# Kernel tuning notes

Hardware: AMD Instinct MI355X
Metric: run time of the kernel (lower is better)

## Reference

```python
import jax, jax.numpy as jnp
import numpy as np

N, T, V = 256, 70, 64
B, H, C = 6, 1024, 4  # n_blocks, n_internal_units, n_class
SPECTRAL_RADIUS = 0.99
INPUT_SCALING = 0.2


def setup_inputs() -> dict:
    key = jax.random.key(0)
    k1, k2, k3, k4 = jax.random.split(key, 4)
    X = jax.random.normal(k1, (N, T, V), dtype=jnp.float32)
    # spectral-radius-normalized reservoir weights (circular law: rho(G/sqrt(H)) ~ 1)
    W_res = jax.random.normal(k2, (B, H, H), dtype=jnp.float32) * (SPECTRAL_RADIUS / jnp.sqrt(H).astype(jnp.float32))
    # +/-1 Bernoulli input weights scaled by input_scaling
    W_in = jnp.sign(jax.random.normal(k3, (B, H, V), dtype=jnp.float32)) * INPUT_SCALING
    W_lin = jax.random.normal(k4, (T, C, B * H), dtype=jnp.float32) * 0.02
    b_lin = jnp.zeros((T, C), dtype=jnp.float32)
    return {"X": X, "W_res": W_res, "W_in": W_in, "W_lin": W_lin, "b_lin": b_lin}


def reference(X, W_res, W_in, W_lin, b_lin):
    # Echo state recurrence: s_t = tanh(W_res @ s_{t-1} + W_in @ x_t), per block
    # (leak=None, noise_level=0.0, n_drop=0 as in module defaults)
    n, t_len, v = X.shape
    b, h, _ = W_res.shape

    def step(s, x_t):  # s: [B,N,H], x_t: [N,V]
        pre = jnp.einsum('bij,bnj->bni', W_res, s) + jnp.einsum('bhv,nv->bnh', W_in, x_t)
        s_new = jnp.tanh(pre)
        return s_new, s_new

    s0 = jnp.zeros((b, n, h), dtype=X.dtype)
    _, states = jax.lax.scan(step, s0, jnp.swapaxes(X, 0, 1))  # [T,B,N,H]

    # per-timestep features: concat blocks -> [T,N,B*H]
    feats = jnp.transpose(states, (0, 2, 1, 3)).reshape(t_len, n, b * h)
    # per-timestep linear heads
    logits = jnp.einsum('tnf,tcf->tnc', feats, W_lin) + b_lin[:, None, :]  # [T,N,C]
    preds = jnp.argmax(logits, axis=-1)  # [T,N], matches forward()'s class_dict
    return logits, preds
```

## Files before the change

### kernel.cpp

```cpp
#include <hip/hip_runtime.h>
#include <stdint.h>


typedef _Float16 f16;
typedef _Float16 f16x8 __attribute__((ext_vector_type(8)));
typedef float floatx4 __attribute__((ext_vector_type(4)));

#define N_TOT 256
#define T_TOT 70
#define V_TOT 64
#define B_TOT 6
#define H_TOT 1024
#define C_TOT 4
#define F_TOT (B_TOT * H_TOT)
#define G_TOT 192
#define LDA 72
#define LO_SCALE 4096.0f
#define LO_INV   (1.0f / 4096.0f)

union H8 { f16 h[8]; uint4 v; };

__global__ __launch_bounds__(256)
void split_f32(const float* __restrict__ src, f16* __restrict__ hi,
               f16* __restrict__ lo, int n)
{
    const int i = (blockIdx.x * 256 + threadIdx.x) * 8;
    if (i + 8 > n) return;
    const float4 a = *(const float4*)&src[i];
    const float4 b = *(const float4*)&src[i + 4];
    const float x[8] = {a.x, a.y, a.z, a.w, b.x, b.y, b.z, b.w};
    H8 H, L;
#pragma unroll
    for (int j = 0; j < 8; ++j) {
        const f16 h = (f16)x[j];
        H.h[j] = h;
        L.h[j] = (f16)((x[j] - (float)h) * LO_SCALE);
    }
    *(uint4*)&hi[i] = H.v;
    *(uint4*)&lo[i] = L.v;
}

__global__ __launch_bounds__(256)
void head_reduce(const float* __restrict__ part,
                 const float* __restrict__ b_lin,
                 float* __restrict__ logits,
                 float* __restrict__ preds)
{
    const int t = blockIdx.x;
    const int n = threadIdx.x;

    float a0 = b_lin[t * C_TOT + 0];
    float a1 = b_lin[t * C_TOT + 1];
    float a2 = b_lin[t * C_TOT + 2];
    float a3 = b_lin[t * C_TOT + 3];

    const float* p = part + (((size_t)t * G_TOT) * N_TOT + n) * C_TOT;
    for (int g = 0; g < G_TOT; ++g) {
        const float4 v = *(const float4*)&p[(size_t)g * N_TOT * C_TOT];
        a0 += v.x; a1 += v.y; a2 += v.z; a3 += v.w;
    }

    float4 o = {a0, a1, a2, a3};
    *(float4*)&logits[((size_t)t * N_TOT + n) * C_TOT] = o;

    int arg = 0;
    float best = a0;
    if (a1 > best) { best = a1; arg = 1; }
    if (a2 > best) { best = a2; arg = 2; }
    if (a3 > best) { best = a3; arg = 3; }
    preds[(size_t)t * N_TOT + n] = (float)arg;
}

__global__ __launch_bounds__(256)
void esn_step_fused(const f16* __restrict__ Xhi,   const f16* __restrict__ Xlo,
                    const f16* __restrict__ Whi,   const f16* __restrict__ Wlo,
                    const f16* __restrict__ Wihi,  const f16* __restrict__ Wilo,
                    const f16* __restrict__ shi_p, const f16* __restrict__ slo_p,
                    f16* __restrict__ shi_n,       f16* __restrict__ slo_n,
                    const float* __restrict__ W_lin, float* __restrict__ part,
                    int t, int first)
{
    __shared__ f16 As_hi[64 * LDA];
    __shared__ f16 As_lo[64 * LDA];
    __shared__ f16 Bs_hi[32 * LDA];
    __shared__ f16 Bs_lo[32 * LDA];

    const int id  = blockIdx.x;
    const int b   = id >> 7;
    const int rem = id & 127;
    const int mt  = rem >> 5;
    const int it  = rem & 31;

    const int tid  = threadIdx.x;
    const int wm   = tid >> 6;
    const int lane = tid & 63;
    const int l16  = lane & 15;
    const int oct  = lane >> 4;

    const int ra = tid >> 2;
    const int ca = (tid & 3) << 4;
    const int rb = tid >> 3;
    const int cb = (tid & 7) << 3;

    floatx4 acc[2], accl[2];
#pragma unroll
    for (int j = 0; j < 2; ++j) { acc[j] = (floatx4)(0.0f); accl[j] = (floatx4)(0.0f); }

    if (!first) {
        const f16* Ah = shi_p + (size_t)(b * N_TOT + mt * 64 + ra) * H_TOT + ca;
        const f16* Al = slo_p + (size_t)(b * N_TOT + mt * 64 + ra) * H_TOT + ca;
        const f16* Bh = Whi   + (size_t)(b * H_TOT + it * 32 + rb) * H_TOT + cb;
        const f16* Bl = Wlo   + (size_t)(b * H_TOT + it * 32 + rb) * H_TOT + cb;

        uint4 pah0, pah1, pal0, pal1, pbh, pbl;
#define LOAD_CHUNK(J0)                                   \
        do {                                             \
            pah0 = *(const uint4*)&Ah[(J0) + 0];         \
            pah1 = *(const uint4*)&Ah[(J0) + 8];         \
            pal0 = *(const uint4*)&Al[(J0) + 0];         \
            pal1 = *(const uint4*)&Al[(J0) + 8];         \
            pbh  = *(const uint4*)&Bh[(J0)];             \
            pbl  = *(const uint4*)&Bl[(J0)];             \
        } while (0)

        LOAD_CHUNK(0);
        for (int kc = 0; kc < 16; ++kc) {
            if (kc) __syncthreads();
            *(uint4*)&As_hi[ra * LDA + ca]     = pah0;
            *(uint4*)&As_hi[ra * LDA + ca + 8] = pah1;
            *(uint4*)&As_lo[ra * LDA + ca]     = pal0;
            *(uint4*)&As_lo[ra * LDA + ca + 8] = pal1;
            *(uint4*)&Bs_hi[rb * LDA + cb]     = pbh;
            *(uint4*)&Bs_lo[rb * LDA + cb]     = pbl;
            __syncthreads();
            if (kc < 15) LOAD_CHUNK((kc + 1) * 64);

#pragma unroll
            for (int kk = 0; kk < 64; kk += 32) {
                const int ar = (wm * 16 + l16) * LDA + kk + oct * 8;
                const f16x8 ah = *(const f16x8*)&As_hi[ar];
                const f16x8 al = *(const f16x8*)&As_lo[ar];
#pragma unroll
                for (int nf = 0; nf < 2; ++nf) {
                    const int br = (nf * 16 + l16) * LDA + kk + oct * 8;
                    const f16x8 bh = *(const f16x8*)&Bs_hi[br];
                    const f16x8 bl = *(const f16x8*)&Bs_lo[br];
                    acc[nf]  = __builtin_amdgcn_mfma_f32_16x16x32_f16(ah, bh, acc[nf], 0, 0, 0);
                    accl[nf] = __builtin_amdgcn_mfma_f32_16x16x32_f16(ah, bl, accl[nf], 0, 0, 0);
                    accl[nf] = __builtin_amdgcn_mfma_f32_16x16x32_f16(al, bh, accl[nf], 0, 0, 0);
                }
            }
        }
#undef LOAD_CHUNK
        __syncthreads();
    }

    {
        const size_t xb = ((size_t)(mt * 64 + ra) * T_TOT + t) * V_TOT + ca;
        *(uint4*)&As_hi[ra * LDA + ca]     = *(const uint4*)&Xhi[xb];
        *(uint4*)&As_hi[ra * LDA + ca + 8] = *(const uint4*)&Xhi[xb + 8];
        *(uint4*)&As_lo[ra * LDA + ca]     = *(const uint4*)&Xlo[xb];
        *(uint4*)&As_lo[ra * LDA + ca + 8] = *(const uint4*)&Xlo[xb + 8];
        const size_t wb = (size_t)(b * H_TOT + it * 32 + rb) * V_TOT + cb;
        *(uint4*)&Bs_hi[rb * LDA + cb] = *(const uint4*)&Wihi[wb];
        *(uint4*)&Bs_lo[rb * LDA + cb] = *(const uint4*)&Wilo[wb];
        __syncthreads();
#pragma unroll
        for (int kk = 0; kk < 64; kk += 32) {
            const int ar = (wm * 16 + l16) * LDA + kk + oct * 8;
            const f16x8 ah = *(const f16x8*)&As_hi[ar];
            const f16x8 al = *(const f16x8*)&As_lo[ar];
#pragma unroll
            for (int nf = 0; nf < 2; ++nf) {
                const int br = (nf * 16 + l16) * LDA + kk + oct * 8;
                const f16x8 bh = *(const f16x8*)&Bs_hi[br];
                const f16x8 bl = *(const f16x8*)&Bs_lo[br];
                acc[nf]  = __builtin_amdgcn_mfma_f32_16x16x32_f16(ah, bh, acc[nf], 0, 0, 0);
                accl[nf] = __builtin_amdgcn_mfma_f32_16x16x32_f16(ah, bl, accl[nf], 0, 0, 0);
                accl[nf] = __builtin_amdgcn_mfma_f32_16x16x32_f16(al, bh, accl[nf], 0, 0, 0);
            }
        }
    }

    const int nbase = mt * 64;
    const int ibase = it * 32;

    const float* wl = W_lin + (size_t)t * C_TOT * F_TOT + b * H_TOT + ibase;
    float w[4][2];
#pragma unroll
    for (int c = 0; c < 4; ++c)
#pragma unroll
        for (int nf = 0; nf < 2; ++nf)
            w[c][nf] = wl[(size_t)c * F_TOT + nf * 16 + l16];

    float sval[2][4];
#pragma unroll
    for (int nf = 0; nf < 2; ++nf)
#pragma unroll
        for (int r = 0; r < 4; ++r) {
            const int m  = wm * 16 + oct * 4 + r;
            const int ii = nf * 16 + l16;
            const float s = tanhf(acc[nf][r] + accl[nf][r] * LO_INV);
            sval[nf][r] = s;
            const f16 h = (f16)s;
            const size_t oidx = (size_t)(b * N_TOT + nbase + m) * H_TOT + ibase + ii;
            shi_n[oidx] = h;
            slo_n[oidx] = (f16)((s - (float)h) * LO_SCALE);
        }

    const int g = b * 32 + it;
#pragma unroll
    for (int r = 0; r < 4; ++r) {
        float v[4];
#pragma unroll
        for (int c = 0; c < 4; ++c) {
            float x = sval[0][r] * w[c][0] + sval[1][r] * w[c][1];
            x += __shfl_xor(x, 1);
            x += __shfl_xor(x, 2);
            x += __shfl_xor(x, 4);
            x += __shfl_xor(x, 8);
            v[c] = x;
        }
        if (l16 == 0) {
            const int n = nbase + wm * 16 + oct * 4 + r;
            float4 o = {v[0], v[1], v[2], v[3]};
            *(float4*)&part[(((size_t)t * G_TOT + g) * N_TOT + n) * C_TOT] = o;
        }
    }
}

extern "C" void kernel_launch(void* const* d_in, const int* in_sizes, int n_in,
                              void* d_out, int out_size, void* d_ws, size_t ws_size,
                              hipStream_t stream) {
    const float* X     = (const float*)d_in[0];
    const float* W_res = (const float*)d_in[1];
    const float* W_in  = (const float*)d_in[2];
    const float* W_lin = (const float*)d_in[3];
    const float* b_lin = (const float*)d_in[4];

    float* out    = (float*)d_out;
    float* logits = out;
    float* preds  = out + (size_t)T_TOT * N_TOT * C_TOT;

    const size_t nWres = (size_t)B_TOT * H_TOT * H_TOT;
    const size_t nWin  = (size_t)B_TOT * H_TOT * V_TOT;
    const size_t nX    = (size_t)N_TOT * T_TOT * V_TOT;
    const size_t nS    = (size_t)B_TOT * N_TOT * H_TOT;
    const size_t nPart = (size_t)T_TOT * G_TOT * N_TOT * C_TOT;

    f16* p    = (f16*)d_ws;
    f16* Whi  = p;  p += nWres;
    f16* Wlo  = p;  p += nWres;
    f16* Wihi = p;  p += nWin;
    f16* Wilo = p;  p += nWin;
    f16* Xhi  = p;  p += nX;
    f16* Xlo  = p;  p += nX;
    f16* sAh  = p;  p += nS;
    f16* sAl  = p;  p += nS;
    f16* sBh  = p;  p += nS;
    f16* sBl  = p;  p += nS;
    float* part = (float*)p;

    split_f32<<<(int)(nWres / 2048), 256, 0, stream>>>(W_res, Whi, Wlo, (int)nWres);
    split_f32<<<(int)(nWin  / 2048), 256, 0, stream>>>(W_in, Wihi, Wilo, (int)nWin);
    split_f32<<<(int)(nX    / 2048), 256, 0, stream>>>(X, Xhi, Xlo, (int)nX);

    for (int t = 0; t < T_TOT; ++t) {
        const f16 *ph, *pl;
        f16 *nh, *nl;
        if (t & 1) { ph = sBh; pl = sBl; nh = sAh; nl = sAl; }
        else       { ph = sAh; pl = sAl; nh = sBh; nl = sBl; }
        esn_step_fused<<<B_TOT * 4 * 32, 256, 0, stream>>>(
            Xhi, Xlo, Whi, Wlo, Wihi, Wilo, ph, pl, nh, nl,
            W_lin, part, t, t == 0 ? 1 : 0);
    }
    head_reduce<<<T_TOT, 256, 0, stream>>>(part, b_lin, logits, preds);
}
```

Baseline: 1.792 ms.

## Load A operands directly to registers and double-buffer B tile in LDS

```diff
diff --git a/kernel.cpp b/kernel.cpp
--- a/kernel.cpp
+++ b/kernel.cpp
@@ -14,11 +14,11 @@
 #define C_TOT 4
 #define F_TOT (B_TOT * H_TOT)
 #define G_TOT 192
-#define LDA 72
+#define LDB 72
 #define LO_SCALE 4096.0f
 #define LO_INV   (1.0f / 4096.0f)
 
-union H8 { f16 h[8]; uint4 v; };
+union H8 { f16 h[8]; uint4 v; f16x8 f; };
 
 __global__ __launch_bounds__(256)
 void split_f32(const float* __restrict__ src, f16* __restrict__ hi,
@@ -71,7 +71,7 @@
     preds[(size_t)t * N_TOT + n] = (float)arg;
 }
 
-__global__ __launch_bounds__(256)
+__global__ __launch_bounds__(256, 3)
 void esn_step_fused(const f16* __restrict__ Xhi,   const f16* __restrict__ Xlo,
                     const f16* __restrict__ Whi,   const f16* __restrict__ Wlo,
                     const f16* __restrict__ Wihi,  const f16* __restrict__ Wilo,
@@ -80,10 +80,8 @@
                     const float* __restrict__ W_lin, float* __restrict__ part,
                     int t, int first)
 {
-    __shared__ f16 As_hi[64 * LDA];
-    __shared__ f16 As_lo[64 * LDA];
-    __shared__ f16 Bs_hi[32 * LDA];
-    __shared__ f16 Bs_lo[32 * LDA];
+    __shared__ f16 Bs_hi[2][32 * LDB];
+    __shared__ f16 Bs_lo[2][32 * LDB];
 
     const int id  = blockIdx.x;
     const int b   = id >> 7;
@@ -97,8 +95,6 @@
     const int l16  = lane & 15;
     const int oct  = lane >> 4;
 
-    const int ra = tid >> 2;
-    const int ca = (tid & 3) << 4;
     const int rb = tid >> 3;
     const int cb = (tid & 7) << 3;
 
@@ -106,79 +102,103 @@
 #pragma unroll
     for (int j = 0; j < 2; ++j) { acc[j] = (floatx4)(0.0f); accl[j] = (floatx4)(0.0f); }
 
+    const int arow = mt * 64 + wm * 16 + l16;
+
+    const f16* Xh = Xhi + ((size_t)arow * T_TOT + t) * V_TOT;
+    const f16* Xl = Xlo + ((size_t)arow * T_TOT + t) * V_TOT;
+    const f16* Bwh = Wihi + (size_t)(b * H_TOT + it * 32 + rb) * V_TOT + cb;
+    const f16* Bwl = Wilo + (size_t)(b * H_TOT + it * 32 + rb) * V_TOT + cb;
+
+    H8 ah0, ah1, al0, al1;
+
     if (!first) {
-        const f16* Ah = shi_p + (size_t)(b * N_TOT + mt * 64 + ra) * H_TOT + ca;
-        const f16* Al = slo_p + (size_t)(b * N_TOT + mt * 64 + ra) * H_TOT + ca;
+        const f16* Ah = shi_p + (size_t)(b * N_TOT + arow) * H_TOT;
+        const f16* Al = slo_p + (size_t)(b * N_TOT + arow) * H_TOT;
         const f16* Bh = Whi   + (size_t)(b * H_TOT + it * 32 + rb) * H_TOT + cb;
         const f16* Bl = Wlo   + (size_t)(b * H_TOT + it * 32 + rb) * H_TOT + cb;
 
-        uint4 pah0, pah1, pal0, pal1, pbh, pbl;
-#define LOAD_CHUNK(J0)                                   \
-        do {                                             \
-            pah0 = *(const uint4*)&Ah[(J0) + 0];         \
-            pah1 = *(const uint4*)&Ah[(J0) + 8];         \
-            pal0 = *(const uint4*)&Al[(J0) + 0];         \
-            pal1 = *(const uint4*)&Al[(J0) + 8];         \
-            pbh  = *(const uint4*)&Bh[(J0)];             \
-            pbl  = *(const uint4*)&Bl[(J0)];             \
-        } while (0)
-
-        LOAD_CHUNK(0);
+        uint4 pbh = *(const uint4*)&Bh[0];
+        uint4 pbl = *(const uint4*)&Bl[0];
+        *(uint4*)&Bs_hi[0][rb * LDB + cb] = pbh;
+        *(uint4*)&Bs_lo[0][rb * LDB + cb] = pbl;
+        pbh = *(const uint4*)&Bh[64];
+        pbl = *(const uint4*)&Bl[64];
+        ah0.v = *(const uint4*)&Ah[oct * 8];
+        ah1.v = *(const uint4*)&Ah[32 + oct * 8];
+        al0.v = *(const uint4*)&Al[oct * 8];
+        al1.v = *(const uint4*)&Al[32 + oct * 8];
+        __syncthreads();
+
         for (int kc = 0; kc < 16; ++kc) {
-            if (kc) __syncthreads();
-            *(uint4*)&As_hi[ra * LDA + ca]     = pah0;
-            *(uint4*)&As_hi[ra * LDA + ca + 8] = pah1;
-            *(uint4*)&As_lo[ra * LDA + ca]     = pal0;
-            *(uint4*)&As_lo[ra * LDA + ca + 8] = pal1;
-            *(uint4*)&Bs_hi[rb * LDA + cb]     = pbh;
-            *(uint4*)&Bs_lo[rb * LDA + cb]     = pbl;
-            __syncthreads();
-            if (kc < 15) LOAD_CHUNK((kc + 1) * 64);
-
-#pragma unroll
-            for (int kk = 0; kk < 64; kk += 32) {
-                const int ar = (wm * 16 + l16) * LDA + kk + oct * 8;
-                const f16x8 ah = *(const f16x8*)&As_hi[ar];
-                const f16x8 al = *(const f16x8*)&As_lo[ar];
+            const int cur = kc & 1;
+
+            *(uint4*)&Bs_hi[cur ^ 1][rb * LDB + cb] = pbh;
+            *(uint4*)&Bs_lo[cur ^ 1][rb * LDB + cb] = pbl;
+            if (kc < 14) {
+                pbh = *(const uint4*)&Bh[(kc + 2) * 64];
+                pbl = *(const uint4*)&Bl[(kc + 2) * 64];
+            } else if (kc == 14) {
+                pbh = *(const uint4*)&Bwh[0];
+                pbl = *(const uint4*)&Bwl[0];
+            }
+
+            H8 nh0, nh1, nl0, nl1;
+            if (kc < 15) {
+                const int ko = (kc + 1) * 64 + oct * 8;
+                nh0.v = *(const uint4*)&Ah[ko];
+                nh1.v = *(const uint4*)&Ah[ko + 32];
+                nl0.v = *(const uint4*)&Al[ko];
+                nl1.v = *(const uint4*)&Al[ko + 32];
+            } else {
+                nh0.v = *(const uint4*)&Xh[oct * 8];
+                nh1.v = *(const uint4*)&Xh[32 + oct * 8];
+                nl0.v = *(const uint4*)&Xl[oct * 8];
+                nl1.v = *(const uint4*)&Xl[32 + oct * 8];
+            }
+
+#pragma unroll
+            for (int half = 0; half < 2; ++half) {
+                const int kk = half * 32;
+                const f16x8 ah = half ? ah1.f : ah0.f;
+                const f16x8 al = half ? al1.f : al0.f;
 #pragma unroll
                 for (int nf = 0; nf < 2; ++nf) {
-                    const int br = (nf * 16 + l16) * LDA + kk + oct * 8;
-                    const f16x8 bh = *(const f16x8*)&Bs_hi[br];
-                    const f16x8 bl = *(const f16x8*)&Bs_lo[br];
+                    const int br = (nf * 16 + l16) * LDB + kk + oct * 8;
+                    const f16x8 bh = *(const f16x8*)&Bs_hi[cur][br];
+                    const f16x8 bl = *(const f16x8*)&Bs_lo[cur][br];
                     acc[nf]  = __builtin_amdgcn_mfma_f32_16x16x32_f16(ah, bh, acc[nf], 0, 0, 0);
                     accl[nf] = __builtin_amdgcn_mfma_f32_16x16x32_f16(ah, bl, accl[nf], 0, 0, 0);
                     accl[nf] = __builtin_amdgcn_mfma_f32_16x16x32_f16(al, bh, accl[nf], 0, 0, 0);
                 }
             }
-        }
-#undef LOAD_CHUNK
+            __syncthreads();
+            ah0 = nh0; ah1 = nh1; al0 = nl0; al1 = nl1;
+        }
+    } else {
+        uint4 pbh = *(const uint4*)&Bwh[0];
+        uint4 pbl = *(const uint4*)&Bwl[0];
+        *(uint4*)&Bs_hi[0][rb * LDB + cb] = pbh;
+        *(uint4*)&Bs_lo[0][rb * LDB + cb] = pbl;
+        ah0.v = *(const uint4*)&Xh[oct * 8];
+        ah1.v = *(const uint4*)&Xh[32 + oct * 8];
+        al0.v = *(const uint4*)&Xl[oct * 8];
+        al1.v = *(const uint4*)&Xl[32 + oct * 8];
         __syncthreads();
     }
 
-    {
-        const size_t xb = ((size_t)(mt * 64 + ra) * T_TOT + t) * V_TOT + ca;
-        *(uint4*)&As_hi[ra * LDA + ca]     = *(const uint4*)&Xhi[xb];
-        *(uint4*)&As_hi[ra * LDA + ca + 8] = *(const uint4*)&Xhi[xb + 8];
-        *(uint4*)&As_lo[ra * LDA + ca]     = *(const uint4*)&Xlo[xb];
-        *(uint4*)&As_lo[ra * LDA + ca + 8] = *(const uint4*)&Xlo[xb + 8];
-        const size_t wb = (size_t)(b * H_TOT + it * 32 + rb) * V_TOT + cb;
-        *(uint4*)&Bs_hi[rb * LDA + cb] = *(const uint4*)&Wihi[wb];
-        *(uint4*)&Bs_lo[rb * LDA + cb] = *(const uint4*)&Wilo[wb];
-        __syncthreads();
-#pragma unroll
-        for (int kk = 0; kk < 64; kk += 32) {
-            const int ar = (wm * 16 + l16) * LDA + kk + oct * 8;
-            const f16x8 ah = *(const f16x8*)&As_hi[ar];
-            const f16x8 al = *(const f16x8*)&As_lo[ar];
-#pragma unroll
-            for (int nf = 0; nf < 2; ++nf) {
-                const int br = (nf * 16 + l16) * LDA + kk + oct * 8;
-                const f16x8 bh = *(const f16x8*)&Bs_hi[br];
-                const f16x8 bl = *(const f16x8*)&Bs_lo[br];
-                acc[nf]  = __builtin_amdgcn_mfma_f32_16x16x32_f16(ah, bh, acc[nf], 0, 0, 0);
-                accl[nf] = __builtin_amdgcn_mfma_f32_16x16x32_f16(ah, bl, accl[nf], 0, 0, 0);
-                accl[nf] = __builtin_amdgcn_mfma_f32_16x16x32_f16(al, bh, accl[nf], 0, 0, 0);
-            }
+#pragma unroll
+    for (int half = 0; half < 2; ++half) {
+        const int kk = half * 32;
+        const f16x8 ah = half ? ah1.f : ah0.f;
+        const f16x8 al = half ? al1.f : al0.f;
+#pragma unroll
+        for (int nf = 0; nf < 2; ++nf) {
+            const int br = (nf * 16 + l16) * LDB + kk + oct * 8;
+            const f16x8 bh = *(const f16x8*)&Bs_hi[0][br];
+            const f16x8 bl = *(const f16x8*)&Bs_lo[0][br];
+            acc[nf]  = __builtin_amdgcn_mfma_f32_16x16x32_f16(ah, bh, acc[nf], 0, 0, 0);
+            accl[nf] = __builtin_amdgcn_mfma_f32_16x16x32_f16(ah, bl, accl[nf], 0, 0, 0);
+            accl[nf] = __builtin_amdgcn_mfma_f32_16x16x32_f16(al, bh, accl[nf], 0, 0, 0);
         }
     }
 
@@ -247,6 +267,7 @@
     const size_t nX    = (size_t)N_TOT * T_TOT * V_TOT;
     const size_t nS    = (size_t)B_TOT * N_TOT * H_TOT;
     const size_t nPart = (size_t)T_TOT * G_TOT * N_TOT * C_TOT;
+    (void)nPart;
 
     f16* p    = (f16*)d_ws;
     f16* Whi  = p;  p += nWres;
```

New measurement: 2.176 ms. 21.5% more time.
